# Kernel optimization log

Measured on AMD Instinct MI355X. Metric: run time of the kernel, lower is better.

## Reference

```python
import jax, jax.numpy as jnp
import numpy as np
from jax import lax

POOL_OUT = 20  # SOCA AdaptiveAvgPool2d((20,20))
MID = 16       # out_channel // 2
BN_EPS = 1e-3


def _pool_matrix(n, out):
    # Row-stochastic matrix replicating torch AdaptiveAvgPool2d bin boundaries:
    # start = floor(i*n/out), end = ceil((i+1)*n/out)
    P = np.zeros((out, n), np.float32)
    for i in range(out):
        s = (i * n) // out
        e = -((-(i + 1) * n) // out)
        P[i, s:e] = 1.0 / (e - s)
    return jnp.asarray(P)


def setup_inputs() -> dict:
    key = jax.random.key(0)
    ks = jax.random.split(key, 5)
    B, C, H, W = 16, 256, 128, 128
    OC = 32
    x = jax.random.normal(ks[0], (B, C, H, W), dtype=jnp.float32)
    linear_w = jax.random.normal(ks[1], (C, C), dtype=jnp.float32) * (1.0 / np.sqrt(C))
    linear_b = jnp.zeros((C,), jnp.float32)
    lsa_w = jax.random.normal(ks[2], (1, 2, 7, 7), dtype=jnp.float32) * 0.1  # Conv2d(2,1,7) no bias
    conv_w = jax.random.normal(ks[3], (OC, OC, 3, 3), dtype=jnp.float32) * (1.0 / np.sqrt(OC * 9))
    conv_b = jnp.zeros((OC,), jnp.float32)
    bn_gamma = jnp.ones((OC,), jnp.float32)
    bn_beta = jnp.zeros((OC,), jnp.float32)
    return {"x": x, "linear_w": linear_w, "linear_b": linear_b, "lsa_w": lsa_w,
            "conv_w": conv_w, "conv_b": conv_b, "bn_gamma": bn_gamma, "bn_beta": bn_beta}


def _bsa_forward(x, linear_w, linear_b, lsa_w, conv_w, conv_b, bn_gamma, bn_beta):
    b, c, h, w = x.shape
    # ---- SOCA: second-order channel attention ----
    PH = _pool_matrix(h, POOL_OUT)
    PW = _pool_matrix(w, POOL_OUT)
    xp = jnp.einsum('oh,bchw,pw->bcop', PH, x, PW)          # (b,c,20,20)
    n = POOL_OUT * POOL_OUT
    v = xp.reshape(b, c, n).transpose(0, 2, 1)               # (b,400,c)
    vc = v - v.mean(axis=1, keepdims=True)
    cov = jnp.einsum('bnc,bnd->bcd', vc, vc) / (n - 1)       # (b,c,c)
    feat = cov.mean(axis=2)                                  # (b,c)
    attn = jax.nn.sigmoid(feat @ linear_w.T + linear_b)      # (b,c)
    # ---- channel scoring / top-k selection ----
    score = attn.mean(axis=0)                                # (c,)
    score_id = jnp.argsort(-score)                           # descending
    max_id = jnp.sort(score_id[:MID])                        # (MID,)
    x1 = jnp.take(x, max_id, axis=1) * (1.0 + score[max_id])[None, :, None, None]
    # ---- grouped channel mean (c divisible by MID by construction) ----
    g = c // MID
    x2 = x.reshape(b, MID, g, h, w).mean(axis=2)             # (b,MID,h,w)
    xc = jnp.concatenate([x1, x2], axis=1)                   # (b,32,h,w)
    # ---- LSA spatial attention ----
    s = jnp.concatenate([xc.mean(axis=1, keepdims=True),
                         xc.max(axis=1, keepdims=True)], axis=1)  # (b,2,h,w)
    a = lax.conv_general_dilated(s, lsa_w, (1, 1), [(3, 3), (3, 3)],
                                 dimension_numbers=('NCHW', 'OIHW', 'NCHW'))
    xa = xc * jax.nn.sigmoid(a)
    # ---- CBA: conv(3x3, stride 2) + BN(train stats) + SiLU ----
    y = lax.conv_general_dilated(xa, conv_w, (2, 2), [(1, 1), (1, 1)],
                                 dimension_numbers=('NCHW', 'OIHW', 'NCHW'))
    y = y + conv_b[None, :, None, None]
    mu = y.mean(axis=(0, 2, 3))
    var = y.var(axis=(0, 2, 3))
    yn = (y - mu[None, :, None, None]) * lax.rsqrt(var + BN_EPS)[None, :, None, None]
    yn = yn * bn_gamma[None, :, None, None] + bn_beta[None, :, None, None]
    return yn * jax.nn.sigmoid(yn)  # SiLU


def reference(x, linear_w, linear_b, lsa_w, conv_w, conv_b, bn_gamma, bn_beta):
    return _bsa_forward(x, linear_w, linear_b, lsa_w, conv_w, conv_b, bn_gamma, bn_beta)
```

## Files before the change

### kernel.cpp

```cpp
#include <hip/hip_runtime.h>
#include <math.h>

#define B_ 16
#define C_ 256
#define H_ 128
#define W_ 128
#define HW_ (H_*W_)
#define PO 20
#define NPOOL (PO*PO)
#define MID_ 16
#define OC_ 32
#define OH_ 64
#define OW_ 64
#define BN_EPS 1e-3f

#define OFF_XP     0
#define OFF_SN     1638400
#define OFF_SCORE  1648896
#define OFF_BNSUM  1649184
#define OFF_BNSQ   1649216
#define OFF_SMEAN  1649248
#define OFF_SMAX   1911392
#define OFF_SIGA   2173536
#define OFF_XC     2435680

__device__ __forceinline__ int bin_s(int p) { return (p * 128) / 20; }
__device__ __forceinline__ int bin_e(int p) { return ((p + 1) * 128 + 19) / 20; }

__global__ __launch_bounds__(256) void k_pool2(const float* __restrict__ x,
                                               float* __restrict__ xp,
                                               float* __restrict__ sn,
                                               float* __restrict__ xc) {
  __shared__ float tmp[2][64 * 21];
  const int blk = blockIdx.x;
  const int b = blk >> 5, g = (blk >> 1) & 15, rh = blk & 1;
  const int tid = threadIdx.x;
  const int hl = tid >> 2, q = tid & 3;
  const int hg = rh * 64 + hl;
  const float* rowbase = x + (size_t)(b * C_) * HW_ + (size_t)hg * W_ + q * 32;

  float4 xacc[8];
#pragma unroll
  for (int j = 0; j < 8; ++j) xacc[j] = make_float4(0.f, 0.f, 0.f, 0.f);
  float snacc = 0.f;

  float4 cur[8], nxt[8];
  {
    const float4* s4 = (const float4*)(rowbase + (size_t)(g * 16) * HW_);
#pragma unroll
    for (int j = 0; j < 8; ++j) cur[j] = s4[j];
  }

#pragma unroll
  for (int k = 0; k < 16; ++k) {
    if (k < 15) {
      const float4* s4 = (const float4*)(rowbase + (size_t)(g * 16 + k + 1) * HW_);
#pragma unroll
      for (int j = 0; j < 8; ++j) nxt[j] = s4[j];
    }
    const int c = g * 16 + k;
    float bin[5];
#pragma unroll
    for (int p = 0; p < 5; ++p) bin[p] = 0.f;
#pragma unroll
    for (int j = 0; j < 8; ++j) {
      float4 v = cur[j];
      xacc[j].x += v.x; xacc[j].y += v.y; xacc[j].z += v.z; xacc[j].w += v.w;
      const float c4[4] = {v.x, v.y, v.z, v.w};
#pragma unroll
      for (int kk = 0; kk < 4; ++kk) {
        const int cc = 4 * j + kk;
#pragma unroll
        for (int p = 0; p < 5; ++p) {
          const int S = (p * 32) / 5;
          const int E = ((p + 1) * 32 + 4) / 5;
          if (cc >= S && cc < E) bin[p] += c4[kk];
        }
      }
    }
    float* tb = tmp[k & 1];
#pragma unroll
    for (int p = 0; p < 5; ++p) {
      const int S = (p * 32) / 5, E = ((p + 1) * 32 + 4) / 5;
      tb[hl * 21 + q * 5 + p] = bin[p] / (float)(E - S);
    }
    asm volatile("s_waitcnt lgkmcnt(0)\n\ts_barrier" ::: "memory");
    if (tid < 200) {
      const int ol = tid / 20, p = tid % 20;
      const int o = rh * 10 + ol;
      const int rs_ = bin_s(o), re_ = bin_e(o);
      float s = 0.f;
      for (int r = rs_; r < re_; ++r) s += tb[(r - rh * 64) * 21 + p];
      float v = s / (float)(re_ - rs_);
      xp[(size_t)(b * C_ + c) * NPOOL + o * PO + p] = v;
      snacc += v;
    }
    if (k < 15) {
#pragma unroll
      for (int j = 0; j < 8; ++j) cur[j] = nxt[j];
    }
  }
  if (tid < 200) atomicAdd(&sn[b * NPOOL + rh * 200 + tid], snacc);
  float4* dst = (float4*)(xc + (size_t)(b * OC_ + MID_ + g) * HW_ + (size_t)hg * W_ + q * 32);
#pragma unroll
  for (int j = 0; j < 8; ++j) {
    float4 v = xacc[j];
    v.x *= 0.0625f; v.y *= 0.0625f; v.z *= 0.0625f; v.w *= 0.0625f;
    dst[j] = v;
  }
}

__global__ __launch_bounds__(256) void k_featattn(const float* __restrict__ xp,
                                                  const float* __restrict__ sn,
                                                  const float* __restrict__ lw,
                                                  const float* __restrict__ lb,
                                                  float* __restrict__ score) {
  const int b = blockIdx.x;
  const int tid = threadIdx.x;
  __shared__ float snl[NPOOL];
  __shared__ float red[256];
  __shared__ float featl[C_];
  for (int i = tid; i < NPOOL; i += 256) snl[i] = sn[b * NPOOL + i];
  __syncthreads();
  const float4* row4 = (const float4*)(xp + (size_t)(b * C_ + tid) * NPOOL);
  float rs = 0.f, dot = 0.f;
#pragma unroll 4
  for (int n = 0; n < NPOOL / 4; ++n) {
    float4 v = row4[n];
    rs += v.x + v.y + v.z + v.w;
    dot += v.x * snl[4 * n] + v.y * snl[4 * n + 1]
         + v.z * snl[4 * n + 2] + v.w * snl[4 * n + 3];
  }
  red[tid] = rs;
  __syncthreads();
  for (int s = 128; s > 0; s >>= 1) {
    if (tid < s) red[tid] += red[tid + s];
    __syncthreads();
  }
  const float totm = red[0] / (float)NPOOL;
  featl[tid] = (dot - totm * rs) / ((float)(NPOOL - 1) * (float)C_);
  __syncthreads();
  const float4* wrow = (const float4*)(lw + (size_t)tid * C_);
  float z = 0.f;
#pragma unroll 4
  for (int i = 0; i < C_ / 4; ++i) {
    float4 w = wrow[i];
    z += w.x * featl[4 * i] + w.y * featl[4 * i + 1]
       + w.z * featl[4 * i + 2] + w.w * featl[4 * i + 3];
  }
  z += lb[tid];
  float sig = 1.0f / (1.0f + expf(-z));
  atomicAdd(&score[tid], sig * (1.0f / (float)B_));
}

__global__ __launch_bounds__(256) void k_build(const float* __restrict__ x,
                                               const float* __restrict__ score,
                                               float* __restrict__ xc,
                                               float* __restrict__ smean,
                                               float* __restrict__ smax) {
  __shared__ float ss[C_];
  __shared__ int flag[C_];
  __shared__ int mid_s[MID_];
  __shared__ float sc_s[MID_];
  __shared__ float4 ps[128], pm[128];
  const int tid = threadIdx.x;
  ss[tid] = score[tid];
  __syncthreads();
  {
    float my = ss[tid];
    int rank = 0;
    for (int k = 0; k < C_; ++k) {
      float v = ss[k];
      rank += (v > my || (v == my && k < tid)) ? 1 : 0;
    }
    flag[tid] = (rank < MID_) ? 1 : 0;
    __syncthreads();
    if (rank < MID_) {
      int pos = 0;
      for (int k = 0; k < tid; ++k) pos += flag[k];
      mid_s[pos] = tid;
      sc_s[pos] = 1.0f + my;
    }
  }
  __syncthreads();
  const int p = tid & 127, s = tid >> 7;
  const int P = blockIdx.x * 128 + p;
  const int b = P >> 12, pix4 = P & 4095;
  const float4* xb = (const float4*)x + (size_t)(b * C_) * (HW_ / 4) + pix4;
  float4* xcb = (float4*)xc + (size_t)(b * OC_) * (HW_ / 4) + pix4;
  float4 ms = make_float4(0.f, 0.f, 0.f, 0.f);
  float4 mx = make_float4(-INFINITY, -INFINITY, -INFINITY, -INFINITY);
#pragma unroll
  for (int mi = 0; mi < 8; ++mi) {
    int m = s * 8 + mi;
    float4 t = xb[(size_t)mid_s[m] * (HW_ / 4)];
    float sc = sc_s[m];
    t.x *= sc; t.y *= sc; t.z *= sc; t.w *= sc;
    xcb[(size_t)m * (HW_ / 4)] = t;
    ms.x += t.x; ms.y += t.y; ms.z += t.z; ms.w += t.w;
    mx.x = fmaxf(mx.x, t.x); mx.y = fmaxf(mx.y, t.y);
    mx.z = fmaxf(mx.z, t.z); mx.w = fmaxf(mx.w, t.w);
  }
#pragma unroll
  for (int gi = 0; gi < 8; ++gi) {
    float4 t = xcb[(size_t)(MID_ + s * 8 + gi) * (HW_ / 4)];
    ms.x += t.x; ms.y += t.y; ms.z += t.z; ms.w += t.w;
    mx.x = fmaxf(mx.x, t.x); mx.y = fmaxf(mx.y, t.y);
    mx.z = fmaxf(mx.z, t.z); mx.w = fmaxf(mx.w, t.w);
  }
  if (s == 1) { ps[p] = ms; pm[p] = mx; }
  __syncthreads();
  if (s == 0) {
    float4 a = ps[p], m2 = pm[p];
    ms.x = (ms.x + a.x) * (1.f / 32.f); ms.y = (ms.y + a.y) * (1.f / 32.f);
    ms.z = (ms.z + a.z) * (1.f / 32.f); ms.w = (ms.w + a.w) * (1.f / 32.f);
    mx.x = fmaxf(mx.x, m2.x); mx.y = fmaxf(mx.y, m2.y);
    mx.z = fmaxf(mx.z, m2.z); mx.w = fmaxf(mx.w, m2.w);
    ((float4*)smean)[P] = ms;
    ((float4*)smax)[P] = mx;
  }
}

__global__ __launch_bounds__(256) void k_lsa(const float* __restrict__ smean,
                                             const float* __restrict__ smax,
                                             const float* __restrict__ lsa_w,
                                             float* __restrict__ siga) {
  __shared__ float w0[49], w1[49];
  if (threadIdx.x < 49) {
    w0[threadIdx.x] = lsa_w[threadIdx.x];
    w1[threadIdx.x] = lsa_w[49 + threadIdx.x];
  }
  __syncthreads();
  int idx = blockIdx.x * 256 + threadIdx.x;
  int b = idx >> 14;
  int pix = idx & (HW_ - 1);
  int h = pix >> 7, w = pix & 127;
  const float* pm = smean + (size_t)b * HW_;
  const float* px = smax + (size_t)b * HW_;
  float acc = 0.f;
  for (int kh = 0; kh < 7; ++kh) {
    int ih = h + kh - 3;
    if (ih < 0 || ih >= H_) continue;
    for (int kw = 0; kw < 7; ++kw) {
      int iw = w + kw - 3;
      if (iw < 0 || iw >= W_) continue;
      int p = ih * W_ + iw;
      acc += pm[p] * w0[kh * 7 + kw] + px[p] * w1[kh * 7 + kw];
    }
  }
  siga[idx] = 1.0f / (1.0f + __expf(-acc));
}

__global__ __launch_bounds__(256) void k_conv(const float* __restrict__ xc,
                                              const float* __restrict__ siga,
                                              const float* __restrict__ conv_w,
                                              const float* __restrict__ conv_b,
                                              float* __restrict__ out,
                                              float* __restrict__ bnsum,
                                              float* __restrict__ bnsq) {
  __shared__ __attribute__((aligned(16))) float in_lds[4 * 5 * 132];
  __shared__ float sg_lds[5 * 132];
  __shared__ float w_lds[288 * 33];
  const int tid = threadIdx.x;
  const int oc = tid & 31;
  const int g = tid >> 5;
  const int b = blockIdx.x >> 5;
  const int oh0 = (blockIdx.x & 31) * 2;
  const int ih0 = 2 * oh0 - 1;

  for (int i = tid; i < 288 * 32; i += 256) {
    int oc_ = i / 288, rem = i % 288;
    w_lds[rem * 33 + oc_] = conv_w[i];
  }
  const float* sgb = siga + (size_t)b * HW_;
  for (int i = tid; i < 5 * 132; i += 256) {
    int r = i / 132, col = i % 132;
    int ih = ih0 + r, iw = col - 1;
    float v = 0.f;
    if (ih >= 0 && ih < H_ && iw >= 0 && iw < W_) v = sgb[ih * W_ + iw];
    sg_lds[i] = v;
  }

  float acc[2][8];
#pragma unroll
  for (int a = 0; a < 2; ++a)
#pragma unroll
    for (int o = 0; o < 8; ++o) acc[a][o] = 0.f;

  for (int chunk = 0; chunk < 8; ++chunk) {
    __syncthreads();
    for (int i = tid; i < 4 * 5 * 132; i += 256) {
      int icl = i / 660;
      int rem = i % 660;
      int r = rem / 132, col = rem % 132;
      int ih = ih0 + r, iw = col - 1;
      float v = 0.f;
      if (ih >= 0 && ih < H_ && iw >= 0 && iw < W_) {
        v = xc[((size_t)(b * OC_) + (chunk * 4 + icl)) * HW_ + ih * W_ + iw] * sg_lds[rem];
      }
      in_lds[i] = v;
    }
    __syncthreads();
#pragma unroll
    for (int icl = 0; icl < 4; ++icl) {
      float wr[9];
      const int wb = (chunk * 4 + icl) * 9 * 33 + oc;
#pragma unroll
      for (int t = 0; t < 9; ++t) wr[t] = w_lds[wb + t * 33];
#pragma unroll
      for (int r = 0; r < 5; ++r) {
        float f[20] __attribute__((aligned(16)));
        const float4* s4 = (const float4*)&in_lds[(icl * 5 + r) * 132 + 16 * g];
#pragma unroll
        for (int j = 0; j < 5; ++j) ((float4*)f)[j] = s4[j];
#pragma unroll
        for (int ohl = 0; ohl < 2; ++ohl) {
          const int kh = r - 2 * ohl;
          if (kh < 0 || kh > 2) continue;
          float w0 = wr[kh * 3 + 0];
          float w1 = wr[kh * 3 + 1];
          float w2 = wr[kh * 3 + 2];
#pragma unroll
          for (int o = 0; o < 8; ++o)
            acc[ohl][o] += f[2 * o] * w0 + f[2 * o + 1] * w1 + f[2 * o + 2] * w2;
        }
      }
    }
  }

  float bias = conv_b[oc];
  float lsum = 0.f, lsq = 0.f;
  float* outp = out + ((size_t)(b * OC_) + oc) * (OH_ * OW_) + (size_t)oh0 * OW_ + g * 8;
#pragma unroll
  for (int ohl = 0; ohl < 2; ++ohl) {
    float vout[8] __attribute__((aligned(16)));
#pragma unroll
    for (int o = 0; o < 8; ++o) {
      float v = acc[ohl][o] + bias;
      vout[o] = v;
      lsum += v;
      lsq += v * v;
    }
    *((float4*)(outp + ohl * OW_)) = *(float4*)&vout[0];
    *((float4*)(outp + ohl * OW_ + 4)) = *(float4*)&vout[4];
  }
  __syncthreads();
  in_lds[tid] = lsum;
  in_lds[256 + tid] = lsq;
  __syncthreads();
  if (tid < 32) {
    float t = 0.f, tq = 0.f;
#pragma unroll
    for (int gg = 0; gg < 8; ++gg) {
      t += in_lds[gg * 32 + tid];
      tq += in_lds[256 + gg * 32 + tid];
    }
    atomicAdd(&bnsum[tid], t);
    atomicAdd(&bnsq[tid], tq);
  }
}

__global__ __launch_bounds__(256) void k_apply(float* __restrict__ out,
                                               const float* __restrict__ sum,
                                               const float* __restrict__ sq,
                                               const float* __restrict__ gamma,
                                               const float* __restrict__ beta) {
  __shared__ float ssc[OC_], ssh[OC_];
  if (threadIdx.x < OC_) {
    int i = threadIdx.x;
    const float N = (float)(B_ * OH_ * OW_);
    float mu = sum[i] / N;
    float var = sq[i] / N - mu * mu;
    float sc = gamma[i] / sqrtf(var + BN_EPS);
    ssc[i] = sc;
    ssh[i] = beta[i] - mu * sc;
  }
  __syncthreads();
  int idx4 = blockIdx.x * 256 + threadIdx.x;
  int oc = (idx4 >> 10) & 31;
  float sc = ssc[oc], sh = ssh[oc];
  float4 v = ((float4*)out)[idx4];
  float t;
  t = v.x * sc + sh; v.x = t / (1.0f + __expf(-t));
  t = v.y * sc + sh; v.y = t / (1.0f + __expf(-t));
  t = v.z * sc + sh; v.z = t / (1.0f + __expf(-t));
  t = v.w * sc + sh; v.w = t / (1.0f + __expf(-t));
  ((float4*)out)[idx4] = v;
}

extern "C" void kernel_launch(void* const* d_in, const int* in_sizes, int n_in,
                              void* d_out, int out_size, void* d_ws, size_t ws_size,
                              hipStream_t stream) {
  const float* x      = (const float*)d_in[0];
  const float* lw     = (const float*)d_in[1];
  const float* lb     = (const float*)d_in[2];
  const float* lsa_w  = (const float*)d_in[3];
  const float* conv_w = (const float*)d_in[4];
  const float* conv_b = (const float*)d_in[5];
  const float* gamma  = (const float*)d_in[6];
  const float* beta   = (const float*)d_in[7];
  float* out = (float*)d_out;
  float* ws = (float*)d_ws;

  hipMemsetAsync(ws + OFF_SN, 0,
                 (size_t)(OFF_BNSQ + OC_ - OFF_SN) * sizeof(float), stream);

  k_pool2<<<512, 256, 0, stream>>>(x, ws + OFF_XP, ws + OFF_SN, ws + OFF_XC);
  k_featattn<<<B_, 256, 0, stream>>>(ws + OFF_XP, ws + OFF_SN, lw, lb, ws + OFF_SCORE);
  k_build<<<512, 256, 0, stream>>>(x, ws + OFF_SCORE, ws + OFF_XC,
                                   ws + OFF_SMEAN, ws + OFF_SMAX);
  k_lsa<<<1024, 256, 0, stream>>>(ws + OFF_SMEAN, ws + OFF_SMAX, lsa_w, ws + OFF_SIGA);
  k_conv<<<512, 256, 0, stream>>>(ws + OFF_XC, ws + OFF_SIGA, conv_w, conv_b, out,
                                  ws + OFF_BNSUM, ws + OFF_BNSQ);
  k_apply<<<2048, 256, 0, stream>>>(out, ws + OFF_BNSUM, ws + OFF_BNSQ, gamma, beta);
}
```

Measured before the change: 504.2 us.

## Raise grid parallelism across pool, feature-attention, build and conv kernels

The pooling kernel now splits rows into quarters and processes two channels at once, combining the group mean through shared memory. It also drops the register double-buffered prefetch. The single 16-block feature/attention kernel is split into two 512-block kernels that use wave shuffles. The build and conv kernels get 1024 blocks with smaller per-block work: conv does one output row per block and loads weights per chunk. The BN atomics are spread over four banks. The aim is to fill more CUs and cut serialized tail kernels, at the cost of more weight reloads and halo reads in conv.

```diff
diff --git a/kernel.cpp b/kernel.cpp
--- a/kernel.cpp
+++ b/kernel.cpp
@@ -17,140 +17,173 @@
 #define OFF_XP     0
 #define OFF_SN     1638400
 #define OFF_SCORE  1648896
+#define OFF_TOTM   1649152
 #define OFF_BNSUM  1649184
-#define OFF_BNSQ   1649216
-#define OFF_SMEAN  1649248
-#define OFF_SMAX   1911392
-#define OFF_SIGA   2173536
-#define OFF_XC     2435680
+#define OFF_BNSQ   1649312
+#define OFF_SMEAN  1649440
+#define OFF_SMAX   1911584
+#define OFF_SIGA   2173728
+#define OFF_XC     2435872
+#define OFF_RS     10824480
+#define OFF_DOT    10828576
 
 __device__ __forceinline__ int bin_s(int p) { return (p * 128) / 20; }
 __device__ __forceinline__ int bin_e(int p) { return ((p + 1) * 128 + 19) / 20; }
 
-__global__ __launch_bounds__(256) void k_pool2(const float* __restrict__ x,
-                                               float* __restrict__ xp,
-                                               float* __restrict__ sn,
-                                               float* __restrict__ xc) {
-  __shared__ float tmp[2][64 * 21];
+__global__ __launch_bounds__(256, 4) void k_pool2(const float* __restrict__ x,
+                                                  float* __restrict__ xp,
+                                                  float* __restrict__ sn,
+                                                  float* __restrict__ xc) {
+  __shared__ float smem[4224];
+  float (*tmp)[2][672] = (float (*)[2][672])smem;
   const int blk = blockIdx.x;
-  const int b = blk >> 5, g = (blk >> 1) & 15, rh = blk & 1;
+  const int b = blk >> 6, g = (blk >> 2) & 15, rq = blk & 3;
   const int tid = threadIdx.x;
-  const int hl = tid >> 2, q = tid & 3;
-  const int hg = rh * 64 + hl;
+  const int kk = tid >> 7, hl = (tid >> 2) & 31, q = tid & 3;
+  const int hg = rq * 32 + hl;
   const float* rowbase = x + (size_t)(b * C_) * HW_ + (size_t)hg * W_ + q * 32;
 
   float4 xacc[8];
 #pragma unroll
   for (int j = 0; j < 8; ++j) xacc[j] = make_float4(0.f, 0.f, 0.f, 0.f);
   float snacc = 0.f;
-
-  float4 cur[8], nxt[8];
-  {
-    const float4* s4 = (const float4*)(rowbase + (size_t)(g * 16) * HW_);
-#pragma unroll
-    for (int j = 0; j < 8; ++j) cur[j] = s4[j];
-  }
-
-#pragma unroll
-  for (int k = 0; k < 16; ++k) {
-    if (k < 15) {
-      const float4* s4 = (const float4*)(rowbase + (size_t)(g * 16 + k + 1) * HW_);
-#pragma unroll
-      for (int j = 0; j < 8; ++j) nxt[j] = s4[j];
-    }
-    const int c = g * 16 + k;
+  const int kk2 = tid / 100, rem = tid % 100, ol = rem / 20, pc = rem % 20;
+  const int o = rq * 5 + ol;
+
+  for (int it = 0; it < 8; ++it) {
+    const int c = g * 16 + 2 * it + kk;
+    const float4* src4 = (const float4*)(rowbase + (size_t)c * HW_);
     float bin[5];
 #pragma unroll
     for (int p = 0; p < 5; ++p) bin[p] = 0.f;
 #pragma unroll
     for (int j = 0; j < 8; ++j) {
-      float4 v = cur[j];
+      float4 v = src4[j];
       xacc[j].x += v.x; xacc[j].y += v.y; xacc[j].z += v.z; xacc[j].w += v.w;
       const float c4[4] = {v.x, v.y, v.z, v.w};
 #pragma unroll
-      for (int kk = 0; kk < 4; ++kk) {
-        const int cc = 4 * j + kk;
+      for (int e = 0; e < 4; ++e) {
+        const int cc = 4 * j + e;
 #pragma unroll
         for (int p = 0; p < 5; ++p) {
           const int S = (p * 32) / 5;
           const int E = ((p + 1) * 32 + 4) / 5;
-          if (cc >= S && cc < E) bin[p] += c4[kk];
+          if (cc >= S && cc < E) bin[p] += c4[e];
         }
       }
     }
-    float* tb = tmp[k & 1];
+    float* tb = tmp[it & 1][kk];
 #pragma unroll
     for (int p = 0; p < 5; ++p) {
       const int S = (p * 32) / 5, E = ((p + 1) * 32 + 4) / 5;
       tb[hl * 21 + q * 5 + p] = bin[p] / (float)(E - S);
     }
-    asm volatile("s_waitcnt lgkmcnt(0)\n\ts_barrier" ::: "memory");
+    __syncthreads();
     if (tid < 200) {
-      const int ol = tid / 20, p = tid % 20;
-      const int o = rh * 10 + ol;
       const int rs_ = bin_s(o), re_ = bin_e(o);
+      const float* tr = tmp[it & 1][kk2];
       float s = 0.f;
-      for (int r = rs_; r < re_; ++r) s += tb[(r - rh * 64) * 21 + p];
+      for (int r = rs_; r < re_; ++r) s += tr[(r - rq * 32) * 21 + pc];
       float v = s / (float)(re_ - rs_);
-      xp[(size_t)(b * C_ + c) * NPOOL + o * PO + p] = v;
+      xp[(size_t)(b * C_ + g * 16 + 2 * it + kk2) * NPOOL + o * PO + pc] = v;
       snacc += v;
     }
-    if (k < 15) {
-#pragma unroll
-      for (int j = 0; j < 8; ++j) cur[j] = nxt[j];
-    }
-  }
-  if (tid < 200) atomicAdd(&sn[b * NPOOL + rh * 200 + tid], snacc);
-  float4* dst = (float4*)(xc + (size_t)(b * OC_ + MID_ + g) * HW_ + (size_t)hg * W_ + q * 32);
-#pragma unroll
-  for (int j = 0; j < 8; ++j) {
-    float4 v = xacc[j];
-    v.x *= 0.0625f; v.y *= 0.0625f; v.z *= 0.0625f; v.w *= 0.0625f;
-    dst[j] = v;
-  }
-}
-
-__global__ __launch_bounds__(256) void k_featattn(const float* __restrict__ xp,
-                                                  const float* __restrict__ sn,
-                                                  const float* __restrict__ lw,
-                                                  const float* __restrict__ lb,
-                                                  float* __restrict__ score) {
-  const int b = blockIdx.x;
-  const int tid = threadIdx.x;
+  }
+  if (tid < 200) atomicAdd(&sn[b * NPOOL + o * PO + pc], snacc);
+  __syncthreads();
+  const int idx = hl * 4 + q;
+  if (kk == 1) {
+#pragma unroll
+    for (int j = 0; j < 8; ++j) {
+      smem[idx * 33 + 4 * j + 0] = xacc[j].x;
+      smem[idx * 33 + 4 * j + 1] = xacc[j].y;
+      smem[idx * 33 + 4 * j + 2] = xacc[j].z;
+      smem[idx * 33 + 4 * j + 3] = xacc[j].w;
+    }
+  }
+  __syncthreads();
+  if (kk == 0) {
+    float4* dst = (float4*)(xc + (size_t)(b * OC_ + MID_ + g) * HW_ + (size_t)hg * W_ + q * 32);
+#pragma unroll
+    for (int j = 0; j < 8; ++j) {
+      float4 v = xacc[j];
+      v.x = (v.x + smem[idx * 33 + 4 * j + 0]) * 0.0625f;
+      v.y = (v.y + smem[idx * 33 + 4 * j + 1]) * 0.0625f;
+      v.z = (v.z + smem[idx * 33 + 4 * j + 2]) * 0.0625f;
+      v.w = (v.w + smem[idx * 33 + 4 * j + 3]) * 0.0625f;
+      dst[j] = v;
+    }
+  }
+}
+
+__global__ __launch_bounds__(256) void k_rsdot(const float* __restrict__ xp,
+                                               const float* __restrict__ sn,
+                                               float* __restrict__ rsb,
+                                               float* __restrict__ dotb,
+                                               float* __restrict__ totm) {
   __shared__ float snl[NPOOL];
-  __shared__ float red[256];
-  __shared__ float featl[C_];
-  for (int i = tid; i < NPOOL; i += 256) snl[i] = sn[b * NPOOL + i];
-  __syncthreads();
-  const float4* row4 = (const float4*)(xp + (size_t)(b * C_ + tid) * NPOOL);
-  float rs = 0.f, dot = 0.f;
-#pragma unroll 4
-  for (int n = 0; n < NPOOL / 4; ++n) {
-    float4 v = row4[n];
-    rs += v.x + v.y + v.z + v.w;
-    dot += v.x * snl[4 * n] + v.y * snl[4 * n + 1]
-         + v.z * snl[4 * n + 2] + v.w * snl[4 * n + 3];
-  }
-  red[tid] = rs;
-  __syncthreads();
-  for (int s = 128; s > 0; s >>= 1) {
-    if (tid < s) red[tid] += red[tid + s];
-    __syncthreads();
-  }
-  const float totm = red[0] / (float)NPOOL;
-  featl[tid] = (dot - totm * rs) / ((float)(NPOOL - 1) * (float)C_);
-  __syncthreads();
-  const float4* wrow = (const float4*)(lw + (size_t)tid * C_);
+  __shared__ float part[8];
+  const int blk = blockIdx.x, tid = threadIdx.x;
+  const int bb = blk >> 5, sub = blk & 31;
+  const int cl = tid >> 5, lane = tid & 31;
+  const int c = sub * 8 + cl;
+  for (int i = tid; i < NPOOL; i += 256) snl[i] = sn[bb * NPOOL + i];
+  __syncthreads();
+  const float* row = xp + (size_t)(bb * C_ + c) * NPOOL;
+  float rs = 0.f, dt = 0.f;
+  for (int n = lane; n < NPOOL; n += 32) {
+    float v = row[n];
+    rs += v;
+    dt += v * snl[n];
+  }
+#pragma unroll
+  for (int o = 16; o > 0; o >>= 1) {
+    rs += __shfl_down(rs, o, 32);
+    dt += __shfl_down(dt, o, 32);
+  }
+  if (lane == 0) {
+    rsb[bb * C_ + c] = rs;
+    dotb[bb * C_ + c] = dt;
+    part[cl] = rs;
+  }
+  __syncthreads();
+  if (tid == 0) {
+    float s = 0.f;
+#pragma unroll
+    for (int i = 0; i < 8; ++i) s += part[i];
+    atomicAdd(&totm[bb], s);
+  }
+}
+
+__global__ __launch_bounds__(256) void k_attn2(const float* __restrict__ rsb,
+                                               const float* __restrict__ dotb,
+                                               const float* __restrict__ totm,
+                                               const float* __restrict__ lw,
+                                               const float* __restrict__ lb,
+                                               float* __restrict__ score) {
+  __shared__ float rs_l[C_], dot_l[C_];
+  const int blk = blockIdx.x, tid = threadIdx.x;
+  const int bb = blk >> 5, sub = blk & 31;
+  rs_l[tid]  = rsb[bb * C_ + tid];
+  dot_l[tid] = dotb[bb * C_ + tid];
+  __syncthreads();
+  const float t = totm[bb] * (1.0f / (float)NPOOL);
+  const int j = sub * 8 + (tid >> 5), lane = tid & 31;
+  const float* wrow = lw + (size_t)j * C_;
+  const float INV = 1.0f / ((float)(NPOOL - 1) * (float)C_);
   float z = 0.f;
-#pragma unroll 4
-  for (int i = 0; i < C_ / 4; ++i) {
-    float4 w = wrow[i];
-    z += w.x * featl[4 * i] + w.y * featl[4 * i + 1]
-       + w.z * featl[4 * i + 2] + w.w * featl[4 * i + 3];
-  }
-  z += lb[tid];
-  float sig = 1.0f / (1.0f + expf(-z));
-  atomicAdd(&score[tid], sig * (1.0f / (float)B_));
+#pragma unroll
+  for (int i0 = 0; i0 < 8; ++i0) {
+    int i = lane + 32 * i0;
+    z += wrow[i] * ((dot_l[i] - t * rs_l[i]) * INV);
+  }
+#pragma unroll
+  for (int o = 16; o > 0; o >>= 1) z += __shfl_down(z, o, 32);
+  if (lane == 0) {
+    float zf = z + lb[j];
+    float sig = 1.0f / (1.0f + expf(-zf));
+    atomicAdd(&score[j], sig * (1.0f / (float)B_));
+  }
 }
 
 __global__ __launch_bounds__(256) void k_build(const float* __restrict__ x,
@@ -162,8 +195,8 @@
   __shared__ int flag[C_];
   __shared__ int mid_s[MID_];
   __shared__ float sc_s[MID_];
-  __shared__ float4 ps[128], pm[128];
-  const int tid = threadIdx.x;
+  __shared__ float4 ps[3 * 64], pm[3 * 64];
+  const int blk = blockIdx.x, tid = threadIdx.x;
   ss[tid] = score[tid];
   __syncthreads();
   {
@@ -183,16 +216,16 @@
     }
   }
   __syncthreads();
-  const int p = tid & 127, s = tid >> 7;
-  const int P = blockIdx.x * 128 + p;
+  const int p = tid & 63, s = tid >> 6;
+  const int P = blk * 64 + p;
   const int b = P >> 12, pix4 = P & 4095;
   const float4* xb = (const float4*)x + (size_t)(b * C_) * (HW_ / 4) + pix4;
   float4* xcb = (float4*)xc + (size_t)(b * OC_) * (HW_ / 4) + pix4;
   float4 ms = make_float4(0.f, 0.f, 0.f, 0.f);
   float4 mx = make_float4(-INFINITY, -INFINITY, -INFINITY, -INFINITY);
 #pragma unroll
-  for (int mi = 0; mi < 8; ++mi) {
-    int m = s * 8 + mi;
+  for (int mi = 0; mi < 4; ++mi) {
+    int m = s * 4 + mi;
     float4 t = xb[(size_t)mid_s[m] * (HW_ / 4)];
     float sc = sc_s[m];
     t.x *= sc; t.y *= sc; t.z *= sc; t.w *= sc;
@@ -202,20 +235,24 @@
     mx.z = fmaxf(mx.z, t.z); mx.w = fmaxf(mx.w, t.w);
   }
 #pragma unroll
-  for (int gi = 0; gi < 8; ++gi) {
-    float4 t = xcb[(size_t)(MID_ + s * 8 + gi) * (HW_ / 4)];
+  for (int gi = 0; gi < 4; ++gi) {
+    float4 t = xcb[(size_t)(MID_ + s * 4 + gi) * (HW_ / 4)];
     ms.x += t.x; ms.y += t.y; ms.z += t.z; ms.w += t.w;
     mx.x = fmaxf(mx.x, t.x); mx.y = fmaxf(mx.y, t.y);
     mx.z = fmaxf(mx.z, t.z); mx.w = fmaxf(mx.w, t.w);
   }
-  if (s == 1) { ps[p] = ms; pm[p] = mx; }
+  if (s > 0) { ps[(s - 1) * 64 + p] = ms; pm[(s - 1) * 64 + p] = mx; }
   __syncthreads();
   if (s == 0) {
-    float4 a = ps[p], m2 = pm[p];
-    ms.x = (ms.x + a.x) * (1.f / 32.f); ms.y = (ms.y + a.y) * (1.f / 32.f);
-    ms.z = (ms.z + a.z) * (1.f / 32.f); ms.w = (ms.w + a.w) * (1.f / 32.f);
-    mx.x = fmaxf(mx.x, m2.x); mx.y = fmaxf(mx.y, m2.y);
-    mx.z = fmaxf(mx.z, m2.z); mx.w = fmaxf(mx.w, m2.w);
+#pragma unroll
+    for (int k = 0; k < 3; ++k) {
+      float4 a = ps[k * 64 + p], m2 = pm[k * 64 + p];
+      ms.x += a.x; ms.y += a.y; ms.z += a.z; ms.w += a.w;
+      mx.x = fmaxf(mx.x, m2.x); mx.y = fmaxf(mx.y, m2.y);
+      mx.z = fmaxf(mx.z, m2.z); mx.w = fmaxf(mx.w, m2.w);
+    }
+    ms.x *= (1.f / 32.f); ms.y *= (1.f / 32.f);
+    ms.z *= (1.f / 32.f); ms.w *= (1.f / 32.f);
     ((float4*)smean)[P] = ms;
     ((float4*)smax)[P] = mx;
   }
@@ -251,29 +288,25 @@
   siga[idx] = 1.0f / (1.0f + __expf(-acc));
 }
 
-__global__ __launch_bounds__(256) void k_conv(const float* __restrict__ xc,
-                                              const float* __restrict__ siga,
-                                              const float* __restrict__ conv_w,
-                                              const float* __restrict__ conv_b,
-                                              float* __restrict__ out,
-                                              float* __restrict__ bnsum,
-                                              float* __restrict__ bnsq) {
-  __shared__ __attribute__((aligned(16))) float in_lds[4 * 5 * 132];
-  __shared__ float sg_lds[5 * 132];
-  __shared__ float w_lds[288 * 33];
+__global__ __launch_bounds__(256, 4) void k_conv(const float* __restrict__ xc,
+                                                 const float* __restrict__ siga,
+                                                 const float* __restrict__ conv_w,
+                                                 const float* __restrict__ conv_b,
+                                                 float* __restrict__ out,
+                                                 float* __restrict__ bnsum,
+                                                 float* __restrict__ bnsq) {
+  __shared__ __attribute__((aligned(16))) float in_lds[4 * 3 * 132];
+  __shared__ float sg_lds[3 * 132];
+  __shared__ float w_lds[4 * 9 * 33];
   const int tid = threadIdx.x;
   const int oc = tid & 31;
   const int g = tid >> 5;
-  const int b = blockIdx.x >> 5;
-  const int oh0 = (blockIdx.x & 31) * 2;
-  const int ih0 = 2 * oh0 - 1;
-
-  for (int i = tid; i < 288 * 32; i += 256) {
-    int oc_ = i / 288, rem = i % 288;
-    w_lds[rem * 33 + oc_] = conv_w[i];
-  }
+  const int b = blockIdx.x >> 6;
+  const int oh = blockIdx.x & 63;
+  const int ih0 = 2 * oh - 1;
+
   const float* sgb = siga + (size_t)b * HW_;
-  for (int i = tid; i < 5 * 132; i += 256) {
+  for (int i = tid; i < 3 * 132; i += 256) {
     int r = i / 132, col = i % 132;
     int ih = ih0 + r, iw = col - 1;
     float v = 0.f;
@@ -281,17 +314,15 @@
     sg_lds[i] = v;
   }
 
-  float acc[2][8];
-#pragma unroll
-  for (int a = 0; a < 2; ++a)
-#pragma unroll
-    for (int o = 0; o < 8; ++o) acc[a][o] = 0.f;
+  float acc[8];
+#pragma unroll
+  for (int o = 0; o < 8; ++o) acc[o] = 0.f;
 
   for (int chunk = 0; chunk < 8; ++chunk) {
     __syncthreads();
-    for (int i = tid; i < 4 * 5 * 132; i += 256) {
-      int icl = i / 660;
-      int rem = i % 660;
+    for (int i = tid; i < 4 * 3 * 132; i += 256) {
+      int icl = i / 396;
+      int rem = i % 396;
       int r = rem / 132, col = rem % 132;
       int ih = ih0 + r, iw = col - 1;
       float v = 0.f;
@@ -300,49 +331,47 @@
       }
       in_lds[i] = v;
     }
+    for (int i = tid; i < 4 * 9 * 32; i += 256) {
+      int oc_ = i & 31, t = i >> 5;
+      int icl = t / 9, k9 = t % 9;
+      w_lds[t * 33 + oc_] = conv_w[(size_t)oc_ * 288 + (chunk * 4 + icl) * 9 + k9];
+    }
     __syncthreads();
 #pragma unroll
     for (int icl = 0; icl < 4; ++icl) {
       float wr[9];
-      const int wb = (chunk * 4 + icl) * 9 * 33 + oc;
-#pragma unroll
-      for (int t = 0; t < 9; ++t) wr[t] = w_lds[wb + t * 33];
-#pragma unroll
-      for (int r = 0; r < 5; ++r) {
+#pragma unroll
+      for (int t = 0; t < 9; ++t) wr[t] = w_lds[(icl * 9 + t) * 33 + oc];
+#pragma unroll
+      for (int r = 0; r < 3; ++r) {
         float f[20] __attribute__((aligned(16)));
-        const float4* s4 = (const float4*)&in_lds[(icl * 5 + r) * 132 + 16 * g];
+        const float4* s4 = (const float4*)&in_lds[(icl * 3 + r) * 132 + 16 * g];
 #pragma unroll
         for (int j = 0; j < 5; ++j) ((float4*)f)[j] = s4[j];
-#pragma unroll
-        for (int ohl = 0; ohl < 2; ++ohl) {
-          const int kh = r - 2 * ohl;
-          if (kh < 0 || kh > 2) continue;
-          float w0 = wr[kh * 3 + 0];
-          float w1 = wr[kh * 3 + 1];
-          float w2 = wr[kh * 3 + 2];
-#pragma unroll
-          for (int o = 0; o < 8; ++o)
-            acc[ohl][o] += f[2 * o] * w0 + f[2 * o + 1] * w1 + f[2 * o + 2] * w2;
-        }
+        float w0 = wr[r * 3 + 0];
+        float w1 = wr[r * 3 + 1];
+        float w2 = wr[r * 3 + 2];
+#pragma unroll
+        for (int o = 0; o < 8; ++o)
+          acc[o] += f[2 * o] * w0 + f[2 * o + 1] * w1 + f[2 * o + 2] * w2;
       }
     }
   }
 
   float bias = conv_b[oc];
   float lsum = 0.f, lsq = 0.f;
-  float* outp = out + ((size_t)(b * OC_) + oc) * (OH_ * OW_) + (size_t)oh0 * OW_ + g * 8;
-#pragma unroll
-  for (int ohl = 0; ohl < 2; ++ohl) {
+  float* outp = out + ((size_t)(b * OC_) + oc) * (OH_ * OW_) + (size_t)oh * OW_ + g * 8;
+  {
     float vout[8] __attribute__((aligned(16)));
 #pragma unroll
     for (int o = 0; o < 8; ++o) {
-      float v = acc[ohl][o] + bias;
+      float v = acc[o] + bias;
       vout[o] = v;
       lsum += v;
       lsq += v * v;
     }
-    *((float4*)(outp + ohl * OW_)) = *(float4*)&vout[0];
-    *((float4*)(outp + ohl * OW_ + 4)) = *(float4*)&vout[4];
+    *((float4*)(outp)) = *(float4*)&vout[0];
+    *((float4*)(outp + 4)) = *(float4*)&vout[4];
   }
   __syncthreads();
   in_lds[tid] = lsum;
@@ -355,8 +384,9 @@
       t += in_lds[gg * 32 + tid];
       tq += in_lds[256 + gg * 32 + tid];
     }
-    atomicAdd(&bnsum[tid], t);
-    atomicAdd(&bnsq[tid], tq);
+    const int bank = (blockIdx.x & 3) * 32;
+    atomicAdd(&bnsum[bank + tid], t);
+    atomicAdd(&bnsq[bank + tid], tq);
   }
 }
 
@@ -369,8 +399,10 @@
   if (threadIdx.x < OC_) {
     int i = threadIdx.x;
     const float N = (float)(B_ * OH_ * OW_);
-    float mu = sum[i] / N;
-    float var = sq[i] / N - mu * mu;
+    float s = sum[i] + sum[32 + i] + sum[64 + i] + sum[96 + i];
+    float q = sq[i] + sq[32 + i] + sq[64 + i] + sq[96 + i];
+    float mu = s / N;
+    float var = q / N - mu * mu;
     float sc = gamma[i] / sqrtf(var + BN_EPS);
     ssc[i] = sc;
     ssh[i] = beta[i] - mu * sc;
@@ -403,14 +435,17 @@
   float* ws = (float*)d_ws;
 
   hipMemsetAsync(ws + OFF_SN, 0,
-                 (size_t)(OFF_BNSQ + OC_ - OFF_SN) * sizeof(float), stream);
-
-  k_pool2<<<512, 256, 0, stream>>>(x, ws + OFF_XP, ws + OFF_SN, ws + OFF_XC);
-  k_featattn<<<B_, 256, 0, stream>>>(ws + OFF_XP, ws + OFF_SN, lw, lb, ws + OFF_SCORE);
-  k_build<<<512, 256, 0, stream>>>(x, ws + OFF_SCORE, ws + OFF_XC,
-                                   ws + OFF_SMEAN, ws + OFF_SMAX);
+                 (size_t)(OFF_BNSQ + 128 - OFF_SN) * sizeof(float), stream);
+
+  k_pool2<<<1024, 256, 0, stream>>>(x, ws + OFF_XP, ws + OFF_SN, ws + OFF_XC);
+  k_rsdot<<<512, 256, 0, stream>>>(ws + OFF_XP, ws + OFF_SN,
+                                   ws + OFF_RS, ws + OFF_DOT, ws + OFF_TOTM);
+  k_attn2<<<512, 256, 0, stream>>>(ws + OFF_RS, ws + OFF_DOT, ws + OFF_TOTM,
+                                   lw, lb, ws + OFF_SCORE);
+  k_build<<<1024, 256, 0, stream>>>(x, ws + OFF_SCORE, ws + OFF_XC,
+                                    ws + OFF_SMEAN, ws + OFF_SMAX);
   k_lsa<<<1024, 256, 0, stream>>>(ws + OFF_SMEAN, ws + OFF_SMAX, lsa_w, ws + OFF_SIGA);
-  k_conv<<<512, 256, 0, stream>>>(ws + OFF_XC, ws + OFF_SIGA, conv_w, conv_b, out,
-                                  ws + OFF_BNSUM, ws + OFF_BNSQ);
+  k_conv<<<1024, 256, 0, stream>>>(ws + OFF_XC, ws + OFF_SIGA, conv_w, conv_b, out,
+                                   ws + OFF_BNSUM, ws + OFF_BNSQ);
   k_apply<<<2048, 256, 0, stream>>>(out, ws + OFF_BNSUM, ws + OFF_BNSQ, gamma, beta);
 }
```

Result: faster. 493.0 us (-2.2%).
